# Kernel tuning notes

Hardware: AMD Instinct MI355X
Metric: run time of the kernel (lower is better)

## Reference

```python
import jax, jax.numpy as jnp
import numpy as np

N = 100000
IN_DIM = 128
HID = 64
OUT = 4


def _gcn_conv(x, W, b, src, dst, deg_inv_sqrt):
    """PyG GCNConv: linear transform, then symmetric-normalized scatter-add.
    src/dst already include self-loops; deg_inv_sqrt precomputed over them."""
    h = x @ W                                   # [N, H]
    norm = deg_inv_sqrt[src] * deg_inv_sqrt[dst]  # [E+N]
    msg = h[src] * norm[:, None]                # gather + scale, [E+N, H]
    out = jax.ops.segment_sum(msg, dst, num_segments=N)  # scatter-add
    return out + b


def setup_inputs() -> dict:
    key = jax.random.key(0)
    ks = jax.random.split(key, 8)
    E = 1600000
    x = jax.random.normal(ks[0], (N, IN_DIM), dtype=jnp.float32)
    edge_index = jax.random.randint(ks[1], (2, E), 0, N, dtype=jnp.int32)
    # Glorot-ish init for weights
    W1 = jax.random.normal(ks[2], (IN_DIM, HID), dtype=jnp.float32) / np.sqrt(IN_DIM)
    b1 = jnp.zeros((HID,), dtype=jnp.float32)
    W2 = jax.random.normal(ks[3], (HID, HID), dtype=jnp.float32) / np.sqrt(HID)
    b2 = jnp.zeros((HID,), dtype=jnp.float32)
    Wfc = jax.random.normal(ks[4], (HID, OUT), dtype=jnp.float32) / np.sqrt(HID)
    bfc = jnp.zeros((OUT,), dtype=jnp.float32)
    return {"x": x, "edge_index": edge_index, "W1": W1, "b1": b1,
            "W2": W2, "b2": b2, "Wfc": Wfc, "bfc": bfc}


def reference(x, edge_index, W1, b1, W2, b2, Wfc, bfc):
    # Add self-loops (GCNConv default add_self_loops=True)
    loops = jnp.arange(N, dtype=edge_index.dtype)
    src = jnp.concatenate([edge_index[0], loops])
    dst = jnp.concatenate([edge_index[1], loops])
    # Symmetric normalization: deg computed at aggregation targets (dst)
    deg = jax.ops.segment_sum(jnp.ones_like(dst, dtype=x.dtype), dst,
                              num_segments=N)
    deg_inv_sqrt = jnp.where(deg > 0, jax.lax.rsqrt(deg), 0.0)

    h = _gcn_conv(x, W1, b1, src, dst, deg_inv_sqrt)
    h = jax.nn.relu(h)                 # dropout is identity in eval mode
    h = _gcn_conv(h, W2, b2, src, dst, deg_inv_sqrt)
    h = jax.nn.relu(h)
    return h @ Wfc + bfc               # [N, 4]
```

## Files before the change

### kernel.cpp

```cpp
#include <hip/hip_runtime.h>
#include <hip/hip_fp16.h>


typedef float v2f __attribute__((ext_vector_type(2)));

__global__ __launch_bounds__(256) void k_bcount(const int* __restrict__ dst, int e,
                                                int* __restrict__ bcnt) {
    __shared__ int lh[512];
    for (int i = threadIdx.x; i < 512; i += 256) lh[i] = 0;
    __syncthreads();
    for (int i = blockIdx.x * blockDim.x + threadIdx.x; i < e;
         i += gridDim.x * blockDim.x)
        atomicAdd(&lh[dst[i] >> 8], 1);
    __syncthreads();
    for (int i = threadIdx.x; i < 512; i += 256)
        if (lh[i]) atomicAdd(&bcnt[i], lh[i]);
}

__global__ __launch_bounds__(512) void k_bscan(const int* __restrict__ bcnt,
                                               int* __restrict__ bbase,
                                               int* __restrict__ bcur) {
    __shared__ int tmp[512];
    int t = threadIdx.x;
    int v = bcnt[t];
    tmp[t] = v;
    __syncthreads();
    for (int o = 1; o < 512; o <<= 1) {
        int x = (t >= o) ? tmp[t - o] : 0;
        __syncthreads();
        tmp[t] += x;
        __syncthreads();
    }
    int ex = tmp[t] - v;
    bbase[t] = ex;
    bcur[t] = ex;
}

__global__ __launch_bounds__(256) void k_bin(const int* __restrict__ src,
                                             const int* __restrict__ dst, int e,
                                             int* bcur, unsigned* __restrict__ binned) {
    __shared__ int lh[512], lbase[512], lr[512];
    int t = threadIdx.x;
    for (int i = t; i < 512; i += 256) { lh[i] = 0; lr[i] = 0; }
    __syncthreads();
    int chunk = (e + gridDim.x - 1) / gridDim.x;
    int lo = blockIdx.x * chunk;
    int hi = min(e, lo + chunk);
    for (int i = lo + t; i < hi; i += 256)
        atomicAdd(&lh[dst[i] >> 8], 1);
    __syncthreads();
    for (int i = t; i < 512; i += 256)
        lbase[i] = lh[i] ? atomicAdd(&bcur[i], lh[i]) : 0;
    __syncthreads();
    for (int i = lo + t; i < hi; i += 256) {
        int d = dst[i];
        int b = d >> 8;
        int r = atomicAdd(&lr[b], 1);
        binned[lbase[b] + r] = ((unsigned)src[i] << 8) | (unsigned)(d & 255);
    }
}

__global__ __launch_bounds__(256) void k_bucket(const unsigned* __restrict__ binned,
                                                const int* __restrict__ bbase,
                                                const int* __restrict__ bcnt,
                                                int n, int* __restrict__ offs,
                                                int* __restrict__ cnt,
                                                float* __restrict__ dis,
                                                int* __restrict__ csr) {
    __shared__ int nh[256], nsc[256], nr[256];
    int b = blockIdx.x, t = threadIdx.x;
    int node0 = b << 8;
    int ebase = bbase[b], ecnt = bcnt[b];
    nh[t] = 0; nr[t] = 0;
    __syncthreads();
    for (int j = t; j < ecnt; j += 256)
        atomicAdd(&nh[binned[ebase + j] & 255u], 1);
    __syncthreads();
    int v = nh[t];
    nsc[t] = v;
    __syncthreads();
    for (int o = 1; o < 256; o <<= 1) {
        int x = (t >= o) ? nsc[t - o] : 0;
        __syncthreads();
        nsc[t] += x;
        __syncthreads();
    }
    int ex = nsc[t] - v;
    int d = node0 + t;
    if (d < n) {
        offs[d] = ebase + ex;
        cnt[d]  = v;
        dis[d]  = rsqrtf((float)(v + 1));
    }
    nsc[t] = ex;
    __syncthreads();
    for (int j = t; j < ecnt; j += 256) {
        unsigned ed = binned[ebase + j];
        int ld = ed & 255u;
        int r = atomicAdd(&nr[ld], 1);
        csr[ebase + nsc[ld] + r] = (int)(ed >> 8);
    }
}

template<int K>
__global__ __launch_bounds__(256) void k_gemm_t(const float* __restrict__ X,
                                                const float* __restrict__ W,
                                                const float* __restrict__ dis,
                                                __half* __restrict__ H, int n) {
    constexpr int BM = 128, CK = 32, XS = BM + 4;
    __shared__ float ws[K * 64];
    __shared__ float xT[CK * XS];

    int t = threadIdx.x;
    for (int i = t; i < K * 16; i += 256)
        ((float4*)ws)[i] = ((const float4*)W)[i];

    int row0 = blockIdx.x * BM;
    int col4 = (t & 15) * 4;
    int row8 = (t >> 4) * 8;
    int kq   = t & 7;
    int rr   = t >> 3;

    v2f acc[8][2] = {};

    for (int kc = 0; kc < K; kc += CK) {
        __syncthreads();
        #pragma unroll
        for (int p = 0; p < 4; ++p) {
            int row  = p * 32 + rr;
            int grow = row0 + row;
            float4 v = make_float4(0.f, 0.f, 0.f, 0.f);
            if (grow < n)
                v = *(const float4*)(X + (size_t)grow * K + kc + kq * 4);
            xT[(kq * 4 + 0) * XS + row] = v.x;
            xT[(kq * 4 + 1) * XS + row] = v.y;
            xT[(kq * 4 + 2) * XS + row] = v.z;
            xT[(kq * 4 + 3) * XS + row] = v.w;
        }
        __syncthreads();
        #pragma unroll
        for (int k = 0; k < CK; ++k) {
            float4 wv  = *(const float4*)(ws + (kc + k) * 64 + col4);
            float4 xv0 = *(const float4*)(xT + k * XS + row8);
            float4 xv1 = *(const float4*)(xT + k * XS + row8 + 4);
            v2f w0 = { wv.x, wv.y };
            v2f w1 = { wv.z, wv.w };
            float xv[8] = { xv0.x, xv0.y, xv0.z, xv0.w,
                            xv1.x, xv1.y, xv1.z, xv1.w };
            #pragma unroll
            for (int i = 0; i < 8; ++i) {
                v2f xs = { xv[i], xv[i] };
                acc[i][0] = __builtin_elementwise_fma(xs, w0, acc[i][0]);
                acc[i][1] = __builtin_elementwise_fma(xs, w1, acc[i][1]);
            }
        }
    }

    #pragma unroll
    for (int i = 0; i < 8; ++i) {
        int grow = row0 + row8 + i;
        if (grow < n) {
            float d = dis[grow];
            union { __half2 h[2]; float2 f; } u;
            u.h[0] = __floats2half2_rn(acc[i][0].x * d, acc[i][0].y * d);
            u.h[1] = __floats2half2_rn(acc[i][1].x * d, acc[i][1].y * d);
            *(float2*)(H + (size_t)grow * 64 + col4) = u.f;
        } else if (grow == n) {
            *(float2*)(H + (size_t)grow * 64 + col4) = make_float2(0.f, 0.f);
        }
    }
}

__device__ inline void add_row(const __half* __restrict__ hp, int s, int c4,
                               v2f& lo, v2f& hi) {
    float2 raw = *(const float2*)(hp + (size_t)s * 64 + c4);
    const __half2* p = (const __half2*)&raw;
    float2 l = __half22float2(p[0]);
    float2 h = __half22float2(p[1]);
    lo += (v2f){ l.x, l.y };
    hi += (v2f){ h.x, h.y };
}

template<bool FUSE>
__global__ __launch_bounds__(256) void k_gather(const __half* __restrict__ hp,
                                                const int* __restrict__ csr,
                                                const int* __restrict__ off,
                                                const int* __restrict__ cnt,
                                                const float* __restrict__ dis,
                                                const float* __restrict__ bias,
                                                float* __restrict__ outb,
                                                const float* __restrict__ Wfc,
                                                const float* __restrict__ bfc,
                                                int n) {
    int lane = threadIdx.x & 63;
    int wid  = (blockIdx.x * blockDim.x + threadIdx.x) >> 6;
    if (wid >= n) return;
    int d    = wid;
    int esub = lane >> 4;
    int c4   = (lane & 15) * 4;

    int start = off[d], num = cnt[d];
    int idx = (lane < num) ? csr[start + lane] : 0;
    int lim = min(num, 64);

    v2f aL[4] = {}, aH[4] = {};
    if (esub == 0)
        add_row(hp, d, c4, aL[0], aH[0]);

    int j = 0;
    for (; j + 16 <= lim; j += 16) {
        int s0 = __shfl(idx, j + esub);
        int s1 = __shfl(idx, j + 4 + esub);
        int s2 = __shfl(idx, j + 8 + esub);
        int s3 = __shfl(idx, j + 12 + esub);
        add_row(hp, s0, c4, aL[0], aH[0]);
        add_row(hp, s1, c4, aL[1], aH[1]);
        add_row(hp, s2, c4, aL[2], aH[2]);
        add_row(hp, s3, c4, aL[3], aH[3]);
    }
    for (; j < lim; j += 4) {
        int jj = j + esub;
        int sr = __shfl(idx, jj);
        int s  = (jj < lim) ? sr : n;
        add_row(hp, s, c4, aL[0], aH[0]);
    }
    for (int j2 = 64; j2 < num; j2 += 4) {
        int jj = j2 + esub;
        if (jj < num) {
            int s = csr[start + jj];
            add_row(hp, s, c4, aL[1], aH[1]);
        }
    }
    v2f sL = (aL[0] + aL[1]) + (aL[2] + aL[3]);
    v2f sH = (aH[0] + aH[1]) + (aH[2] + aH[3]);
    float4 a0 = make_float4(sL.x, sL.y, sH.x, sH.y);
    #pragma unroll
    for (int o = 16; o <= 32; o <<= 1) {
        a0.x += __shfl_xor(a0.x, o);
        a0.y += __shfl_xor(a0.y, o);
        a0.z += __shfl_xor(a0.z, o);
        a0.w += __shfl_xor(a0.w, o);
    }
    float dd = dis[d];
    float4 bb = *(const float4*)(bias + c4);
    float4 o;
    o.x = fmaxf(bb.x + dd * a0.x, 0.f);
    o.y = fmaxf(bb.y + dd * a0.y, 0.f);
    o.z = fmaxf(bb.z + dd * a0.z, 0.f);
    o.w = fmaxf(bb.w + dd * a0.w, 0.f);
    if (!FUSE) {
        if (esub == 0)
            *(float4*)(outb + (size_t)d * 64 + c4) = o;
    } else {
        const float4* W4 = (const float4*)Wfc;
        float4 w0 = W4[c4 + 0], w1 = W4[c4 + 1], w2 = W4[c4 + 2], w3 = W4[c4 + 3];
        float4 p;
        p.x = o.x * w0.x + o.y * w1.x + o.z * w2.x + o.w * w3.x;
        p.y = o.x * w0.y + o.y * w1.y + o.z * w2.y + o.w * w3.y;
        p.z = o.x * w0.z + o.y * w1.z + o.z * w2.z + o.w * w3.z;
        p.w = o.x * w0.w + o.y * w1.w + o.z * w2.w + o.w * w3.w;
        #pragma unroll
        for (int q = 1; q <= 8; q <<= 1) {
            p.x += __shfl_xor(p.x, q);
            p.y += __shfl_xor(p.y, q);
            p.z += __shfl_xor(p.z, q);
            p.w += __shfl_xor(p.w, q);
        }
        if (lane == 0) {
            float4 bf = *(const float4*)bfc;
            float4 r = make_float4(p.x + bf.x, p.y + bf.y, p.z + bf.z, p.w + bf.w);
            ((float4*)outb)[d] = r;
        }
    }
}

static inline size_t align256(size_t x) { return (x + 255) & ~(size_t)255; }

extern "C" void kernel_launch(void* const* d_in, const int* in_sizes, int n_in,
                              void* d_out, int out_size, void* d_ws, size_t ws_size,
                              hipStream_t stream) {
    const float* x   = (const float*)d_in[0];
    const int*   ei  = (const int*)d_in[1];
    const float* W1  = (const float*)d_in[2];
    const float* b1  = (const float*)d_in[3];
    const float* W2  = (const float*)d_in[4];
    const float* b2  = (const float*)d_in[5];
    const float* Wfc = (const float*)d_in[6];
    const float* bfc = (const float*)d_in[7];
    float* out = (float*)d_out;

    int n = in_sizes[0] / 128;
    int e = in_sizes[1] / 2;
    const int* src = ei;
    const int* dst = ei + e;

    char* ws = (char*)d_ws;
    size_t p = 0;
    float*  dis    = (float*) (ws + p); p = align256(p + (size_t)n * 4);
    int*    counts = (int*)   (ws + p); p = align256(p + (size_t)n * 4);
    int*    offs   = (int*)   (ws + p); p = align256(p + (size_t)n * 4);
    int*    bcnt   = (int*)   (ws + p); p = align256(p + 512 * 4);
    int*    bbase  = (int*)   (ws + p); p = align256(p + 512 * 4);
    int*    bcur   = (int*)   (ws + p); p = align256(p + 512 * 4);
    int*    csr    = (int*)   (ws + p); p = align256(p + (size_t)e * 4);
    __half* hbuf   = (__half*)(ws + p); p = align256(p + (size_t)(n + 1) * 64 * 2);
    float*  a1     = (float*) (ws + p);
    unsigned* binned = (unsigned*)a1;

    int gb  = (n + 127) / 128;
    int nbk = (n + 255) / 256;

    hipMemsetAsync(bcnt, 0, 512 * sizeof(int), stream);
    k_bcount<<<256, 256, 0, stream>>>(dst, e, bcnt);
    k_bscan<<<1, 512, 0, stream>>>(bcnt, bbase, bcur);
    k_bin<<<256, 256, 0, stream>>>(src, dst, e, bcur, binned);
    k_bucket<<<nbk, 256, 0, stream>>>(binned, bbase, bcnt, n, offs, counts, dis, csr);

    k_gemm_t<128><<<gb, 256, 0, stream>>>(x, W1, dis, hbuf, n);
    k_gather<false><<<(n * 64 + 255) / 256, 256, 0, stream>>>(
        hbuf, csr, offs, counts, dis, b1, a1, nullptr, nullptr, n);

    k_gemm_t<64><<<gb, 256, 0, stream>>>(a1, W2, dis, hbuf, n);
    k_gather<true><<<(n * 64 + 255) / 256, 256, 0, stream>>>(
        hbuf, csr, offs, counts, dis, b2, out, Wfc, bfc, n);
}
```

Before: 296.7 us.

## Use fp16 MFMA for feature transforms and store layer-1 output in half

Replaces the scalar FMA tiled GEMM with a matrix-core kernel that converts X and W tiles to fp16 in shared memory and uses 16x16x32 f16 MFMA instructions. The first gather now writes its activations as fp16 instead of fp32, halving that intermediate's write and read traffic. The second GEMM consumes those half inputs directly. Binned edges get their own workspace region, and the padding row is zeroed with a memset. The cost is lower input precision (fp16 inputs with fp32 accumulation) and scalar 2-byte output stores in the GEMM epilogue.

```diff
diff --git a/kernel.cpp b/kernel.cpp
--- a/kernel.cpp
+++ b/kernel.cpp
@@ -3,6 +3,8 @@
 
 
 typedef float v2f __attribute__((ext_vector_type(2)));
+typedef _Float16 f16x8 __attribute__((ext_vector_type(8)));
+typedef float f32x4 __attribute__((ext_vector_type(4)));
 
 __global__ __launch_bounds__(256) void k_bcount(const int* __restrict__ dst, int e,
                                                 int* __restrict__ bcnt) {
@@ -102,73 +104,82 @@
     }
 }
 
-template<int K>
-__global__ __launch_bounds__(256) void k_gemm_t(const float* __restrict__ X,
-                                                const float* __restrict__ W,
-                                                const float* __restrict__ dis,
-                                                __half* __restrict__ H, int n) {
-    constexpr int BM = 128, CK = 32, XS = BM + 4;
-    __shared__ float ws[K * 64];
-    __shared__ float xT[CK * XS];
+template<int K, typename TI>
+__global__ __launch_bounds__(256) void k_gemm_mfma(const TI* __restrict__ X,
+                                                   const float* __restrict__ W,
+                                                   const float* __restrict__ dis,
+                                                   __half* __restrict__ Hh, int n) {
+    constexpr int KP = K + 8;
+    __shared__ _Float16 As[64 * KP];
+    __shared__ _Float16 Bs[64 * KP];
 
     int t = threadIdx.x;
-    for (int i = t; i < K * 16; i += 256)
-        ((float4*)ws)[i] = ((const float4*)W)[i];
-
-    int row0 = blockIdx.x * BM;
-    int col4 = (t & 15) * 4;
-    int row8 = (t >> 4) * 8;
-    int kq   = t & 7;
-    int rr   = t >> 3;
-
-    v2f acc[8][2] = {};
-
-    for (int kc = 0; kc < K; kc += CK) {
-        __syncthreads();
-        #pragma unroll
-        for (int p = 0; p < 4; ++p) {
-            int row  = p * 32 + rr;
-            int grow = row0 + row;
+    _Float16* H = (_Float16*)Hh;
+
+    for (int i = t; i < K * 64; i += 256) {
+        int k = i >> 6, nn = i & 63;
+        Bs[nn * KP + k] = (_Float16)W[i];
+    }
+
+    int row0  = blockIdx.x * 64;
+    int rowIn = t >> 2;
+    int seg   = t & 3;
+    int grow  = row0 + rowIn;
+    constexpr int PER = K / 4;
+    if (sizeof(TI) == 4) {
+        const float* Xf = (const float*)X;
+        #pragma unroll
+        for (int q = 0; q < PER / 4; ++q) {
             float4 v = make_float4(0.f, 0.f, 0.f, 0.f);
             if (grow < n)
-                v = *(const float4*)(X + (size_t)grow * K + kc + kq * 4);
-            xT[(kq * 4 + 0) * XS + row] = v.x;
-            xT[(kq * 4 + 1) * XS + row] = v.y;
-            xT[(kq * 4 + 2) * XS + row] = v.z;
-            xT[(kq * 4 + 3) * XS + row] = v.w;
-        }
-        __syncthreads();
-        #pragma unroll
-        for (int k = 0; k < CK; ++k) {
-            float4 wv  = *(const float4*)(ws + (kc + k) * 64 + col4);
-            float4 xv0 = *(const float4*)(xT + k * XS + row8);
-            float4 xv1 = *(const float4*)(xT + k * XS + row8 + 4);
-            v2f w0 = { wv.x, wv.y };
-            v2f w1 = { wv.z, wv.w };
-            float xv[8] = { xv0.x, xv0.y, xv0.z, xv0.w,
-                            xv1.x, xv1.y, xv1.z, xv1.w };
-            #pragma unroll
-            for (int i = 0; i < 8; ++i) {
-                v2f xs = { xv[i], xv[i] };
-                acc[i][0] = __builtin_elementwise_fma(xs, w0, acc[i][0]);
-                acc[i][1] = __builtin_elementwise_fma(xs, w1, acc[i][1]);
-            }
-        }
-    }
-
+                v = *(const float4*)(Xf + (size_t)grow * K + seg * PER + q * 4);
+            __half2* dsts = (__half2*)(As + rowIn * KP + seg * PER + q * 4);
+            dsts[0] = __floats2half2_rn(v.x, v.y);
+            dsts[1] = __floats2half2_rn(v.z, v.w);
+        }
+    } else {
+        const __half* Xh = (const __half*)X;
+        #pragma unroll
+        for (int q = 0; q < PER / 4; ++q) {
+            float2 raw = make_float2(0.f, 0.f);
+            if (grow < n)
+                raw = *(const float2*)(Xh + (size_t)grow * K + seg * PER + q * 4);
+            *(float2*)(As + rowIn * KP + seg * PER + q * 4) = raw;
+        }
+    }
+    __syncthreads();
+
+    int wv   = t >> 6;
+    int lane = t & 63;
+    int m    = lane & 15;
+    int quad = lane >> 4;
+    int r0   = wv * 16;
+
+    f32x4 acc[4] = {};
+    const _Float16* Arow = As + (r0 + m) * KP + quad * 8;
     #pragma unroll
-    for (int i = 0; i < 8; ++i) {
-        int grow = row0 + row8 + i;
-        if (grow < n) {
-            float d = dis[grow];
-            union { __half2 h[2]; float2 f; } u;
-            u.h[0] = __floats2half2_rn(acc[i][0].x * d, acc[i][0].y * d);
-            u.h[1] = __floats2half2_rn(acc[i][1].x * d, acc[i][1].y * d);
-            *(float2*)(H + (size_t)grow * 64 + col4) = u.f;
-        } else if (grow == n) {
-            *(float2*)(H + (size_t)grow * 64 + col4) = make_float2(0.f, 0.f);
-        }
-    }
+    for (int kb = 0; kb < K / 32; ++kb) {
+        f16x8 af = *(const f16x8*)(Arow + kb * 32);
+        #pragma unroll
+        for (int nt = 0; nt < 4; ++nt) {
+            f16x8 bf = *(const f16x8*)(Bs + (nt * 16 + m) * KP + quad * 8 + kb * 32);
+            acc[nt] = __builtin_amdgcn_mfma_f32_16x16x32_f16(af, bf, acc[nt], 0, 0, 0);
+        }
+    }
+
+    float dv[4];
+    int   gr[4];
+    #pragma unroll
+    for (int r = 0; r < 4; ++r) {
+        gr[r] = row0 + r0 + quad * 4 + r;
+        dv[r] = (gr[r] < n) ? dis[gr[r]] : 0.f;
+    }
+    #pragma unroll
+    for (int nt = 0; nt < 4; ++nt)
+        #pragma unroll
+        for (int r = 0; r < 4; ++r)
+            if (gr[r] < n)
+                H[(size_t)gr[r] * 64 + nt * 16 + m] = (_Float16)(acc[nt][r] * dv[r]);
 }
 
 __device__ inline void add_row(const __half* __restrict__ hp, int s, int c4,
@@ -188,7 +199,7 @@
                                                 const int* __restrict__ cnt,
                                                 const float* __restrict__ dis,
                                                 const float* __restrict__ bias,
-                                                float* __restrict__ outb,
+                                                void* __restrict__ outb,
                                                 const float* __restrict__ Wfc,
                                                 const float* __restrict__ bfc,
                                                 int n) {
@@ -249,8 +260,12 @@
     o.z = fmaxf(bb.z + dd * a0.z, 0.f);
     o.w = fmaxf(bb.w + dd * a0.w, 0.f);
     if (!FUSE) {
-        if (esub == 0)
-            *(float4*)(outb + (size_t)d * 64 + c4) = o;
+        if (esub == 0) {
+            union { __half2 h[2]; float2 f; } u;
+            u.h[0] = __floats2half2_rn(o.x, o.y);
+            u.h[1] = __floats2half2_rn(o.z, o.w);
+            *(float2*)((__half*)outb + (size_t)d * 64 + c4) = u.f;
+        }
     } else {
         const float4* W4 = (const float4*)Wfc;
         float4 w0 = W4[c4 + 0], w1 = W4[c4 + 1], w2 = W4[c4 + 2], w3 = W4[c4 + 3];
@@ -296,31 +311,32 @@
 
     char* ws = (char*)d_ws;
     size_t p = 0;
-    float*  dis    = (float*) (ws + p); p = align256(p + (size_t)n * 4);
-    int*    counts = (int*)   (ws + p); p = align256(p + (size_t)n * 4);
-    int*    offs   = (int*)   (ws + p); p = align256(p + (size_t)n * 4);
-    int*    bcnt   = (int*)   (ws + p); p = align256(p + 512 * 4);
-    int*    bbase  = (int*)   (ws + p); p = align256(p + 512 * 4);
-    int*    bcur   = (int*)   (ws + p); p = align256(p + 512 * 4);
-    int*    csr    = (int*)   (ws + p); p = align256(p + (size_t)e * 4);
-    __half* hbuf   = (__half*)(ws + p); p = align256(p + (size_t)(n + 1) * 64 * 2);
-    float*  a1     = (float*) (ws + p);
-    unsigned* binned = (unsigned*)a1;
-
-    int gb  = (n + 127) / 128;
+    float*    dis    = (float*)   (ws + p); p = align256(p + (size_t)n * 4);
+    int*      counts = (int*)     (ws + p); p = align256(p + (size_t)n * 4);
+    int*      offs   = (int*)     (ws + p); p = align256(p + (size_t)n * 4);
+    int*      bcnt   = (int*)     (ws + p); p = align256(p + 512 * 4);
+    int*      bbase  = (int*)     (ws + p); p = align256(p + 512 * 4);
+    int*      bcur   = (int*)     (ws + p); p = align256(p + 512 * 4);
+    int*      csr    = (int*)     (ws + p); p = align256(p + (size_t)e * 4);
+    unsigned* binned = (unsigned*)(ws + p); p = align256(p + (size_t)e * 4);
+    __half*   hbuf   = (__half*)  (ws + p); p = align256(p + (size_t)(n + 1) * 64 * 2);
+    __half*   a1h    = (__half*)  (ws + p);
+
+    int gb  = (n + 63) / 64;
     int nbk = (n + 255) / 256;
 
     hipMemsetAsync(bcnt, 0, 512 * sizeof(int), stream);
+    hipMemsetAsync(hbuf + (size_t)n * 64, 0, 64 * sizeof(__half), stream);
     k_bcount<<<256, 256, 0, stream>>>(dst, e, bcnt);
     k_bscan<<<1, 512, 0, stream>>>(bcnt, bbase, bcur);
     k_bin<<<256, 256, 0, stream>>>(src, dst, e, bcur, binned);
     k_bucket<<<nbk, 256, 0, stream>>>(binned, bbase, bcnt, n, offs, counts, dis, csr);
 
-    k_gemm_t<128><<<gb, 256, 0, stream>>>(x, W1, dis, hbuf, n);
+    k_gemm_mfma<128, float><<<gb, 256, 0, stream>>>(x, W1, dis, hbuf, n);
     k_gather<false><<<(n * 64 + 255) / 256, 256, 0, stream>>>(
-        hbuf, csr, offs, counts, dis, b1, a1, nullptr, nullptr, n);
-
-    k_gemm_t<64><<<gb, 256, 0, stream>>>(a1, W2, dis, hbuf, n);
+        hbuf, csr, offs, counts, dis, b1, a1h, nullptr, nullptr, n);
+
+    k_gemm_mfma<64, __half><<<gb, 256, 0, stream>>>(a1h, W2, dis, hbuf, n);
     k_gather<true><<<(n * 64 + 255) / 256, 256, 0, stream>>>(
         hbuf, csr, offs, counts, dis, b2, out, Wfc, bfc, n);
 }
```

New measurement: 284.1 us. 4.3% less time.
